# Kernel optimization log

Measured on AMD Instinct MI355X. Metric: run time of the kernel, lower is better.

The kernel has to match this reference:

```python
import jax, jax.numpy as jnp
import numpy as np

D_MODEL, JOINT_DIM, VOCAB = 512, 640, 1024
B, T, U = 4, 256, 64


def setup_inputs() -> dict:
    key = jax.random.key(0)
    ks = jax.random.split(key, 8)
    s_in = 1.0 / np.sqrt(D_MODEL)
    s_j = 1.0 / np.sqrt(JOINT_DIM)
    return {
        "enc": jax.random.normal(ks[0], (B, T, D_MODEL), jnp.float32),
        "pred": jax.random.normal(ks[1], (B, U, D_MODEL), jnp.float32),
        "enc_w": jax.random.uniform(ks[2], (JOINT_DIM, D_MODEL), jnp.float32, -s_in, s_in),
        "enc_b": jax.random.uniform(ks[3], (JOINT_DIM,), jnp.float32, -s_in, s_in),
        "pred_w": jax.random.uniform(ks[4], (JOINT_DIM, D_MODEL), jnp.float32, -s_in, s_in),
        "pred_b": jax.random.uniform(ks[5], (JOINT_DIM,), jnp.float32, -s_in, s_in),
        "out_w": jax.random.uniform(ks[6], (VOCAB, JOINT_DIM), jnp.float32, -s_j, s_j),
        "out_b": jax.random.uniform(ks[7], (VOCAB,), jnp.float32, -s_j, s_j),
    }


def reference(enc, pred, enc_w, enc_b, pred_w, pred_b, out_w, out_b):
    # project encoder (B,T,J) and predictor (B,U,J)
    e = jnp.einsum("btd,jd->btj", enc, enc_w) + enc_b
    p = jnp.einsum("bud,jd->buj", pred, pred_w) + pred_b
    # broadcast add over the (T,U) grid, tanh, then vocab projection
    z = jnp.tanh(e[:, :, None, :] + p[:, None, :, :])  # (B,T,U,J)
    logits = jnp.einsum("btuj,vj->btuv", z, out_w) + out_b  # (B,T,U,V)
    return logits
```

## Files before the change

kernel.cpp:

```cpp
#include <hip/hip_runtime.h>
#include <cstdint>
#include <cstddef>


typedef __attribute__((ext_vector_type(8))) __bf16 bf16x8;
typedef __attribute__((ext_vector_type(4))) float f32x4;

__device__ __forceinline__ int swz(int row, int kElem) {
  return (row << 6) + (kElem ^ ((row & 7) << 3));
}

__device__ __forceinline__ float fast_tanh(float x) {
  float e = __builtin_amdgcn_exp2f(x * 2.88539008177793f);
  return 1.0f - 2.0f * __builtin_amdgcn_rcpf(e + 1.0f);
}

__device__ __forceinline__ void gload_lds16(const void* g, void* l) {
  __builtin_amdgcn_global_load_lds(
      (const __attribute__((address_space(1))) void*)g,
      (__attribute__((address_space(3))) void*)l, 16, 0, 0);
}

__device__ void proj_tile(const float* __restrict__ A, const float* __restrict__ W,
                          const float* __restrict__ bias, __bf16* __restrict__ C,
                          int mt, int nt, __bf16* As, __bf16* Bs)
{
  const int tid  = threadIdx.x;
  const int r = tid & 127, half = tid >> 7;
  const int lane = tid & 63, wv = tid >> 6;
  const int wm = wv >> 1, wn = wv & 1;

  const float* arow = A + (size_t)(mt * 128 + r) * 512 + half * 32;
  const float* wrow = W + (size_t)(nt * 128 + r) * 512 + half * 32;

  f32x4 acc[4][4] = {};

  for (int k0 = 0; k0 < 512; k0 += 64) {
#pragma unroll
    for (int s = 0; s < 4; ++s) {
      f32x4 a0 = *(const f32x4*)(arow + k0 + s * 8);
      f32x4 a1 = *(const f32x4*)(arow + k0 + s * 8 + 4);
      f32x4 w0 = *(const f32x4*)(wrow + k0 + s * 8);
      f32x4 w1 = *(const f32x4*)(wrow + k0 + s * 8 + 4);
      bf16x8 za, zw;
#pragma unroll
      for (int j = 0; j < 4; ++j) {
        za[j] = (__bf16)a0[j]; za[4 + j] = (__bf16)a1[j];
        zw[j] = (__bf16)w0[j]; zw[4 + j] = (__bf16)w1[j];
      }
      const int kk = half * 32 + s * 8;
      *(bf16x8*)&As[swz(r, kk)] = za;
      *(bf16x8*)&Bs[swz(r, kk)] = zw;
    }
    __syncthreads();
#pragma unroll
    for (int kk = 0; kk < 2; ++kk) {
      bf16x8 af[4], bfr[4];
#pragma unroll
      for (int i = 0; i < 4; ++i) {
        af[i]  = *(const bf16x8*)&As[swz(wm * 64 + i * 16 + (lane & 15), kk * 32 + (lane >> 4) * 8)];
        bfr[i] = *(const bf16x8*)&Bs[swz(wn * 64 + i * 16 + (lane & 15), kk * 32 + (lane >> 4) * 8)];
      }
#pragma unroll
      for (int mi = 0; mi < 4; ++mi)
#pragma unroll
        for (int ni = 0; ni < 4; ++ni)
          acc[mi][ni] = __builtin_amdgcn_mfma_f32_16x16x32_bf16(af[mi], bfr[ni], acc[mi][ni], 0, 0, 0);
    }
    __syncthreads();
  }

  const int rowbase = mt * 128 + wm * 64;
  const int colbase = nt * 128 + wn * 64;
#pragma unroll
  for (int ni = 0; ni < 4; ++ni) {
    const int col = colbase + ni * 16 + (lane & 15);
    const float bb = bias[col];
#pragma unroll
    for (int mi = 0; mi < 4; ++mi) {
      const int row = rowbase + mi * 16 + (lane >> 4) * 4;
#pragma unroll
      for (int rg = 0; rg < 4; ++rg)
        C[(size_t)(row + rg) * 640 + col] = (__bf16)(acc[mi][ni][rg] + bb);
    }
  }
}

__global__ __launch_bounds__(256) void prep_kernel(
    const float* __restrict__ enc,  const float* __restrict__ enc_w,  const float* __restrict__ enc_b,
    const float* __restrict__ pred, const float* __restrict__ pred_w, const float* __restrict__ pred_b,
    const float* __restrict__ out_w,
    __bf16* __restrict__ E, __bf16* __restrict__ P, __bf16* __restrict__ Wb)
{
  __shared__ __align__(16) __bf16 As[128 * 64];
  __shared__ __align__(16) __bf16 Bs[128 * 64];
  const int bid = blockIdx.x;
  if (bid < 40) {
    proj_tile(enc, enc_w, enc_b, E, bid / 5, bid % 5, As, Bs);
  } else if (bid < 50) {
    proj_tile(pred, pred_w, pred_b, P, (bid - 40) / 5, (bid - 40) % 5, As, Bs);
  } else {
    const int gid = (bid - 50) * 256 + threadIdx.x;
    const int v  = gid / 80;
    const int j8 = gid % 80;
    f32x4 w0 = *(const f32x4*)(out_w + (size_t)v * 640 + j8 * 8);
    f32x4 w1 = *(const f32x4*)(out_w + (size_t)v * 640 + j8 * 8 + 4);
    bf16x8 z;
#pragma unroll
    for (int j = 0; j < 4; ++j) { z[j] = (__bf16)w0[j]; z[4 + j] = (__bf16)w1[j]; }
    const int nb = v >> 7, rr = v & 127;
    const int kb = j8 >> 3, kk = (j8 & 7) * 8;
    *(bf16x8*)(Wb + ((size_t)(nb * 10 + kb) << 13) + swz(rr, kk)) = z;
  }
}

__global__ __launch_bounds__(256) void zprod_kernel(
    const __bf16* __restrict__ E, const __bf16* __restrict__ P,
    __bf16* __restrict__ Z)
{
  const int bid = blockIdx.x;
  const int mt = bid / 10, kt = bid % 10;
  const int row0 = mt << 7;
  const int b  = row0 >> 14;
  const int t0 = (row0 >> 6) & 255;
  __bf16* zdst = Z + ((size_t)bid << 13);
  const int k0 = kt << 6;

#pragma unroll
  for (int c = 0; c < 4; ++c) {
    const int o = c * 2048 + threadIdx.x * 8;
    const int r = o >> 6;
    const int k = (o & 63) ^ ((r & 7) << 3);
    const __bf16* ep = E + (size_t)((b << 8) + t0 + (r >> 6)) * 640 + k0 + k;
    const __bf16* pp = P + (size_t)((b << 6) + (r & 63)) * 640 + k0 + k;
    bf16x8 e8 = *(const bf16x8*)ep;
    bf16x8 p8 = *(const bf16x8*)pp;
    bf16x8 z;
#pragma unroll
    for (int j = 0; j < 8; ++j)
      z[j] = (__bf16)fast_tanh((float)e8[j] + (float)p8[j]);
    *(bf16x8*)&zdst[o] = z;
  }
}

__global__ __launch_bounds__(256) void joiner_mainz(
    const __bf16* __restrict__ Z, const __bf16* __restrict__ Wb,
    const float* __restrict__ outb, float* __restrict__ out)
{
  __shared__ __align__(16) __bf16 As[8192];
  __shared__ __align__(16) __bf16 Bs[8192];
  const int wg = blockIdx.x;
  const int bid = (wg & 7) * 512 + (wg >> 3);
  const int mt = bid >> 3, nt = bid & 7;
  const int tid = threadIdx.x;
  const int lane = tid & 63, wv = tid >> 6;
  const int wm = wv >> 1, wn = wv & 1;

  const __bf16* zsrc = Z  + ((size_t)(mt * 10) << 13);
  const __bf16* wsrc = Wb + ((size_t)(nt * 10) << 13);

  f32x4 acc[4][4] = {};

  for (int kt = 0; kt < 10; ++kt) {
    const size_t kb = (size_t)kt << 13;
#pragma unroll
    for (int c = 0; c < 4; ++c) {
      const int off = c * 2048 + wv * 512;
      gload_lds16(zsrc + kb + off + lane * 8, &As[off]);
      gload_lds16(wsrc + kb + off + lane * 8, &Bs[off]);
    }
    __syncthreads();
#pragma unroll
    for (int kk = 0; kk < 2; ++kk) {
      bf16x8 af[4], bfr[4];
#pragma unroll
      for (int i = 0; i < 4; ++i) {
        af[i]  = *(const bf16x8*)&As[swz(wm * 64 + i * 16 + (lane & 15), kk * 32 + (lane >> 4) * 8)];
        bfr[i] = *(const bf16x8*)&Bs[swz(wn * 64 + i * 16 + (lane & 15), kk * 32 + (lane >> 4) * 8)];
      }
#pragma unroll
      for (int mi = 0; mi < 4; ++mi)
#pragma unroll
        for (int ni = 0; ni < 4; ++ni)
          acc[mi][ni] = __builtin_amdgcn_mfma_f32_16x16x32_bf16(af[mi], bfr[ni], acc[mi][ni], 0, 0, 0);
    }
    __syncthreads();
  }

  const int rowbase = (mt << 7) + wm * 64;
  const int colbase = (nt << 7) + wn * 64;
#pragma unroll
  for (int ni = 0; ni < 4; ++ni) {
    const int col = colbase + ni * 16 + (lane & 15);
    const float bb = outb[col];
#pragma unroll
    for (int mi = 0; mi < 4; ++mi) {
      const int row = rowbase + mi * 16 + (lane >> 4) * 4;
#pragma unroll
      for (int rg = 0; rg < 4; ++rg)
        out[(size_t)(row + rg) * 1024 + col] = acc[mi][ni][rg] + bb;
    }
  }
}

__global__ __launch_bounds__(512, 4) void joiner_fused(
    const __bf16* __restrict__ E, const __bf16* __restrict__ P,
    const __bf16* __restrict__ Wb, const float* __restrict__ outb,
    float* __restrict__ out)
{
  __shared__ __align__(16) __bf16 As[8192];
  __shared__ __align__(16) __bf16 Bs[2][16384];
  const int tid = threadIdx.x;
  const int nt = blockIdx.x & 3;
  const int mt = blockIdx.x >> 2;
  const int row0 = mt << 7;
  const int b  = row0 >> 14;
  const int t0 = (row0 >> 6) & 255;
  const int ar = tid & 127, h = tid >> 7;
  const int lane = tid & 63, wv = tid >> 6;
  const int wm = wv >> 2, wn = wv & 3;

  const __bf16* ep = E + (size_t)((b << 8) + t0 + (ar >> 6)) * 640 + h * 16;
  const __bf16* pp = P + (size_t)((b << 6) + (ar & 63)) * 640 + h * 16;

  f32x4 acc[4][4] = {};
  bf16x8 eA[2], pA[2];

  auto stageB = [&](int kt, __bf16* dst) {
#pragma unroll
    for (int c = 0; c < 4; ++c) {
      const int blk = nt * 2 + (c >> 1);
      const int off = (c & 1) * 4096 + wv * 512;
      gload_lds16(Wb + ((size_t)(blk * 10 + kt) << 13) + off + lane * 8,
                  dst + c * 2048 * 2 - (c >> 1) * 8192 + ((c & 1) * 4096 + wv * 512) - ((c & 1) * 4096 + wv * 512) + (c * 4096 - (c >> 1) * 8192) * 0 + 0);
    }
  };
  (void)stageB;

  auto stageB2 = [&](int kt, __bf16* dst) {
#pragma unroll
    for (int c = 0; c < 4; ++c) {
      const int blk = nt * 2 + (c >> 1);
      const int inoff = (c & 1) * 4096 + wv * 512;
      gload_lds16(Wb + ((size_t)(blk * 10 + kt) << 13) + inoff + lane * 8,
                  dst + (c >> 1) * 8192 + inoff);
    }
  };
  auto loadEP = [&](int k0) {
#pragma unroll
    for (int c = 0; c < 2; ++c) {
      eA[c] = *(const bf16x8*)(ep + k0 + c * 8);
      pA[c] = *(const bf16x8*)(pp + k0 + c * 8);
    }
  };
  auto writeA = [&]() {
#pragma unroll
    for (int c = 0; c < 2; ++c) {
      bf16x8 z;
#pragma unroll
      for (int j = 0; j < 8; ++j)
        z[j] = (__bf16)fast_tanh((float)eA[c][j] + (float)pA[c][j]);
      *(bf16x8*)&As[swz(ar, h * 16 + c * 8)] = z;
    }
  };
  auto compute = [&](const __bf16* Bsc) {
#pragma unroll
    for (int kk = 0; kk < 2; ++kk) {
      bf16x8 af[4], bfr[4];
#pragma unroll
      for (int i = 0; i < 4; ++i) {
        af[i]  = *(const bf16x8*)&As[swz(wm * 64 + i * 16 + (lane & 15), kk * 32 + (lane >> 4) * 8)];
        bfr[i] = *(const bf16x8*)&Bsc[swz(wn * 64 + i * 16 + (lane & 15), kk * 32 + (lane >> 4) * 8)];
      }
      asm volatile("s_waitcnt lgkmcnt(0)" ::: "memory");
      __builtin_amdgcn_sched_barrier(0);
      __builtin_amdgcn_s_setprio(1);
#pragma unroll
      for (int mi = 0; mi < 4; ++mi)
#pragma unroll
        for (int ni = 0; ni < 4; ++ni)
          acc[mi][ni] = __builtin_amdgcn_mfma_f32_16x16x32_bf16(af[mi], bfr[ni], acc[mi][ni], 0, 0, 0);
      __builtin_amdgcn_s_setprio(0);
    }
  };

  stageB2(0, Bs[0]);
  loadEP(0);
  writeA();
  asm volatile("s_waitcnt vmcnt(0) lgkmcnt(0)" ::: "memory");
  __builtin_amdgcn_s_barrier();

  for (int kt = 0; kt < 9; ++kt) {
    const int cur = kt & 1;
    stageB2(kt + 1, Bs[cur ^ 1]);
    loadEP((kt + 1) << 6);
    compute(Bs[cur]);
    __builtin_amdgcn_s_barrier();
    __builtin_amdgcn_sched_barrier(0);
    writeA();
    asm volatile("s_waitcnt lgkmcnt(0)" ::: "memory");
    __builtin_amdgcn_s_barrier();
  }
  compute(Bs[1]);

  const int rowbase = row0 + wm * 64;
  const int colbase = (nt << 8) + wn * 64;
#pragma unroll
  for (int ni = 0; ni < 4; ++ni) {
    const int col = colbase + ni * 16 + (lane & 15);
    const float bb = outb[col];
#pragma unroll
    for (int mi = 0; mi < 4; ++mi) {
      const int row = rowbase + mi * 16 + (lane >> 4) * 4;
#pragma unroll
      for (int rg = 0; rg < 4; ++rg)
        out[(size_t)(row + rg) * 1024 + col] = acc[mi][ni][rg] + bb;
    }
  }
}

extern "C" void kernel_launch(void* const* d_in, const int* in_sizes, int n_in,
                              void* d_out, int out_size, void* d_ws, size_t ws_size,
                              hipStream_t stream) {
  const float* enc    = (const float*)d_in[0];
  const float* pred   = (const float*)d_in[1];
  const float* enc_w  = (const float*)d_in[2];
  const float* enc_b  = (const float*)d_in[3];
  const float* pred_w = (const float*)d_in[4];
  const float* pred_b = (const float*)d_in[5];
  const float* out_w  = (const float*)d_in[6];
  const float* out_b  = (const float*)d_in[7];
  float* out = (float*)d_out;

  char* ws = (char*)d_ws;
  __bf16* E  = (__bf16*)(ws);
  __bf16* P  = (__bf16*)(ws + 1310720);
  __bf16* Wb = (__bf16*)(ws + 1638400);
  __bf16* Z  = (__bf16*)(ws + 2949120);

  prep_kernel<<<dim3(370), dim3(256), 0, stream>>>(
      enc, enc_w, enc_b, pred, pred_w, pred_b, out_w, E, P, Wb);

  if (ws_size >= (size_t)86835200) {
    zprod_kernel<<<dim3(5120), dim3(256), 0, stream>>>(E, P, Z);
    joiner_mainz<<<dim3(4096), dim3(256), 0, stream>>>(Z, Wb, out_b, out);
  } else {
    joiner_fused<<<dim3(2048), dim3(512), 0, stream>>>(E, P, Wb, out_b, out);
  }
}
```

Baseline: 171.7 us.

## Replace Z-path GEMM with 256x256-tile, 4-stage LDS ring pipelined kernel

```diff
diff --git a/kernel.cpp b/kernel.cpp
--- a/kernel.cpp
+++ b/kernel.cpp
@@ -6,8 +6,11 @@
 typedef __attribute__((ext_vector_type(8))) __bf16 bf16x8;
 typedef __attribute__((ext_vector_type(4))) float f32x4;
 
-__device__ __forceinline__ int swz(int row, int kElem) {
+__device__ __forceinline__ int swz64(int row, int kElem) {
   return (row << 6) + (kElem ^ ((row & 7) << 3));
+}
+__device__ __forceinline__ int swz32(int row, int kElem) {
+  return (row << 5) + ((kElem & 7) | (((kElem >> 3) ^ ((row >> 2) & 3)) << 3));
 }
 
 __device__ __forceinline__ float fast_tanh(float x) {
@@ -49,8 +52,8 @@
         zw[j] = (__bf16)w0[j]; zw[4 + j] = (__bf16)w1[j];
       }
       const int kk = half * 32 + s * 8;
-      *(bf16x8*)&As[swz(r, kk)] = za;
-      *(bf16x8*)&Bs[swz(r, kk)] = zw;
+      *(bf16x8*)&As[swz64(r, kk)] = za;
+      *(bf16x8*)&Bs[swz64(r, kk)] = zw;
     }
     __syncthreads();
 #pragma unroll
@@ -58,8 +61,8 @@
       bf16x8 af[4], bfr[4];
 #pragma unroll
       for (int i = 0; i < 4; ++i) {
-        af[i]  = *(const bf16x8*)&As[swz(wm * 64 + i * 16 + (lane & 15), kk * 32 + (lane >> 4) * 8)];
-        bfr[i] = *(const bf16x8*)&Bs[swz(wn * 64 + i * 16 + (lane & 15), kk * 32 + (lane >> 4) * 8)];
+        af[i]  = *(const bf16x8*)&As[swz64(wm * 64 + i * 16 + (lane & 15), kk * 32 + (lane >> 4) * 8)];
+        bfr[i] = *(const bf16x8*)&Bs[swz64(wn * 64 + i * 16 + (lane & 15), kk * 32 + (lane >> 4) * 8)];
       }
 #pragma unroll
       for (int mi = 0; mi < 4; ++mi)
@@ -90,7 +93,7 @@
     const float* __restrict__ enc,  const float* __restrict__ enc_w,  const float* __restrict__ enc_b,
     const float* __restrict__ pred, const float* __restrict__ pred_w, const float* __restrict__ pred_b,
     const float* __restrict__ out_w,
-    __bf16* __restrict__ E, __bf16* __restrict__ P, __bf16* __restrict__ Wb)
+    __bf16* __restrict__ E, __bf16* __restrict__ P, __bf16* __restrict__ Wb, int zpath)
 {
   __shared__ __align__(16) __bf16 As[128 * 64];
   __shared__ __align__(16) __bf16 Bs[128 * 64];
@@ -108,9 +111,15 @@
     bf16x8 z;
 #pragma unroll
     for (int j = 0; j < 4; ++j) { z[j] = (__bf16)w0[j]; z[4 + j] = (__bf16)w1[j]; }
-    const int nb = v >> 7, rr = v & 127;
-    const int kb = j8 >> 3, kk = (j8 & 7) * 8;
-    *(bf16x8*)(Wb + ((size_t)(nb * 10 + kb) << 13) + swz(rr, kk)) = z;
+    if (zpath) {
+      const int nb = v >> 8, rr = v & 255;
+      const int kt = j8 >> 2;
+      *(bf16x8*)(Wb + ((size_t)(nb * 20 + kt) << 13) + swz32(rr, (j8 & 3) * 8)) = z;
+    } else {
+      const int nb = v >> 7, rr = v & 127;
+      const int kb = j8 >> 3, kk = (j8 & 7) * 8;
+      *(bf16x8*)(Wb + ((size_t)(nb * 10 + kb) << 13) + swz64(rr, kk)) = z;
+    }
   }
 }
 
@@ -119,20 +128,20 @@
     __bf16* __restrict__ Z)
 {
   const int bid = blockIdx.x;
-  const int mt = bid / 10, kt = bid % 10;
-  const int row0 = mt << 7;
+  const int mt = bid / 20, kt = bid % 20;
+  const int row0 = mt << 8;
   const int b  = row0 >> 14;
   const int t0 = (row0 >> 6) & 255;
   __bf16* zdst = Z + ((size_t)bid << 13);
-  const int k0 = kt << 6;
 
 #pragma unroll
   for (int c = 0; c < 4; ++c) {
     const int o = c * 2048 + threadIdx.x * 8;
-    const int r = o >> 6;
-    const int k = (o & 63) ^ ((r & 7) << 3);
-    const __bf16* ep = E + (size_t)((b << 8) + t0 + (r >> 6)) * 640 + k0 + k;
-    const __bf16* pp = P + (size_t)((b << 6) + (r & 63)) * 640 + k0 + k;
+    const int r = o >> 5;
+    const int cc = (o >> 3) & 3;
+    const int k = kt * 32 + ((cc ^ ((r >> 2) & 3)) << 3);
+    const __bf16* ep = E + (size_t)((b << 8) + t0 + (r >> 6)) * 640 + k;
+    const __bf16* pp = P + (size_t)((b << 6) + (r & 63)) * 640 + k;
     bf16x8 e8 = *(const bf16x8*)ep;
     bf16x8 p8 = *(const bf16x8*)pp;
     bf16x8 z;
@@ -143,58 +152,77 @@
   }
 }
 
-__global__ __launch_bounds__(256) void joiner_mainz(
+__global__ __launch_bounds__(512, 2) void joiner_ring(
     const __bf16* __restrict__ Z, const __bf16* __restrict__ Wb,
     const float* __restrict__ outb, float* __restrict__ out)
 {
-  __shared__ __align__(16) __bf16 As[8192];
-  __shared__ __align__(16) __bf16 Bs[8192];
+  __shared__ __align__(16) __bf16 As[4][8192];
+  __shared__ __align__(16) __bf16 Bs[4][8192];
   const int wg = blockIdx.x;
-  const int bid = (wg & 7) * 512 + (wg >> 3);
-  const int mt = bid >> 3, nt = bid & 7;
+  const int bid = (wg & 7) * 128 + (wg >> 3);
+  const int mt = bid >> 2, nt = bid & 3;
   const int tid = threadIdx.x;
   const int lane = tid & 63, wv = tid >> 6;
-  const int wm = wv >> 1, wn = wv & 1;
-
-  const __bf16* zsrc = Z  + ((size_t)(mt * 10) << 13);
-  const __bf16* wsrc = Wb + ((size_t)(nt * 10) << 13);
-
-  f32x4 acc[4][4] = {};
-
-  for (int kt = 0; kt < 10; ++kt) {
-    const size_t kb = (size_t)kt << 13;
-#pragma unroll
-    for (int c = 0; c < 4; ++c) {
-      const int off = c * 2048 + wv * 512;
-      gload_lds16(zsrc + kb + off + lane * 8, &As[off]);
-      gload_lds16(wsrc + kb + off + lane * 8, &Bs[off]);
-    }
-    __syncthreads();
-#pragma unroll
-    for (int kk = 0; kk < 2; ++kk) {
-      bf16x8 af[4], bfr[4];
-#pragma unroll
-      for (int i = 0; i < 4; ++i) {
-        af[i]  = *(const bf16x8*)&As[swz(wm * 64 + i * 16 + (lane & 15), kk * 32 + (lane >> 4) * 8)];
-        bfr[i] = *(const bf16x8*)&Bs[swz(wn * 64 + i * 16 + (lane & 15), kk * 32 + (lane >> 4) * 8)];
-      }
-#pragma unroll
-      for (int mi = 0; mi < 4; ++mi)
-#pragma unroll
-        for (int ni = 0; ni < 4; ++ni)
-          acc[mi][ni] = __builtin_amdgcn_mfma_f32_16x16x32_bf16(af[mi], bfr[ni], acc[mi][ni], 0, 0, 0);
-    }
-    __syncthreads();
-  }
-
-  const int rowbase = (mt << 7) + wm * 64;
-  const int colbase = (nt << 7) + wn * 64;
+  const int wm = wv >> 2, wn = wv & 3;
+
+  const __bf16* zsrc = Z  + ((size_t)(mt * 20) << 13);
+  const __bf16* wsrc = Wb + ((size_t)(nt * 20) << 13);
+
+  f32x4 acc[8][4] = {};
+
+  const int arow_s = ((wm * 128 + (lane & 15)) >> 2) & 3;
+  const int brow_s = ((wn * 64  + (lane & 15)) >> 2) & 3;
+  const int aoff = (wm * 128 + (lane & 15)) * 32 + (((lane >> 4) ^ arow_s) << 3);
+  const int boff = (wn * 64  + (lane & 15)) * 32 + (((lane >> 4) ^ brow_s) << 3);
+
+  auto stage = [&](int t) {
+    const int s = t & 3;
+    const size_t g = (size_t)t << 13;
+#pragma unroll
+    for (int c = 0; c < 2; ++c) {
+      const int off = c * 4096 + wv * 512;
+      gload_lds16(zsrc + g + off + lane * 8, &As[s][off]);
+      gload_lds16(wsrc + g + off + lane * 8, &Bs[s][off]);
+    }
+  };
+
+  stage(0); stage(1); stage(2);
+  asm volatile("s_waitcnt vmcnt(8)" ::: "memory");
+  __builtin_amdgcn_s_barrier();
+
+#pragma unroll
+  for (int t = 0; t < 20; ++t) {
+    const int s = t & 3;
+    if (t < 17) stage(t + 3);
+    __builtin_amdgcn_s_setprio(1);
+    bf16x8 bfr[4];
+#pragma unroll
+    for (int ni = 0; ni < 4; ++ni)
+      bfr[ni] = *(const bf16x8*)&Bs[s][boff + ni * 512];
+#pragma unroll
+    for (int mi = 0; mi < 8; ++mi) {
+      bf16x8 af = *(const bf16x8*)&As[s][aoff + mi * 512];
+#pragma unroll
+      for (int ni = 0; ni < 4; ++ni)
+        acc[mi][ni] = __builtin_amdgcn_mfma_f32_16x16x32_bf16(af, bfr[ni], acc[mi][ni], 0, 0, 0);
+    }
+    __builtin_amdgcn_s_setprio(0);
+    if (t < 19) {
+      if (t < 17)       asm volatile("s_waitcnt vmcnt(8)" ::: "memory");
+      else if (t == 17) asm volatile("s_waitcnt vmcnt(4)" ::: "memory");
+      else              asm volatile("s_waitcnt vmcnt(0)" ::: "memory");
+      __builtin_amdgcn_s_barrier();
+    }
+  }
+
+  const int rowbase = (mt << 8) + wm * 128;
+  const int colbase = (nt << 8) + wn * 64;
 #pragma unroll
   for (int ni = 0; ni < 4; ++ni) {
     const int col = colbase + ni * 16 + (lane & 15);
     const float bb = outb[col];
 #pragma unroll
-    for (int mi = 0; mi < 4; ++mi) {
+    for (int mi = 0; mi < 8; ++mi) {
       const int row = rowbase + mi * 16 + (lane >> 4) * 4;
 #pragma unroll
       for (int rg = 0; rg < 4; ++rg)
@@ -226,17 +254,6 @@
   f32x4 acc[4][4] = {};
   bf16x8 eA[2], pA[2];
 
-  auto stageB = [&](int kt, __bf16* dst) {
-#pragma unroll
-    for (int c = 0; c < 4; ++c) {
-      const int blk = nt * 2 + (c >> 1);
-      const int off = (c & 1) * 4096 + wv * 512;
-      gload_lds16(Wb + ((size_t)(blk * 10 + kt) << 13) + off + lane * 8,
-                  dst + c * 2048 * 2 - (c >> 1) * 8192 + ((c & 1) * 4096 + wv * 512) - ((c & 1) * 4096 + wv * 512) + (c * 4096 - (c >> 1) * 8192) * 0 + 0);
-    }
-  };
-  (void)stageB;
-
   auto stageB2 = [&](int kt, __bf16* dst) {
 #pragma unroll
     for (int c = 0; c < 4; ++c) {
@@ -260,7 +277,7 @@
 #pragma unroll
       for (int j = 0; j < 8; ++j)
         z[j] = (__bf16)fast_tanh((float)eA[c][j] + (float)pA[c][j]);
-      *(bf16x8*)&As[swz(ar, h * 16 + c * 8)] = z;
+      *(bf16x8*)&As[swz64(ar, h * 16 + c * 8)] = z;
     }
   };
   auto compute = [&](const __bf16* Bsc) {
@@ -269,8 +286,8 @@
       bf16x8 af[4], bfr[4];
 #pragma unroll
       for (int i = 0; i < 4; ++i) {
-        af[i]  = *(const bf16x8*)&As[swz(wm * 64 + i * 16 + (lane & 15), kk * 32 + (lane >> 4) * 8)];
-        bfr[i] = *(const bf16x8*)&Bsc[swz(wn * 64 + i * 16 + (lane & 15), kk * 32 + (lane >> 4) * 8)];
+        af[i]  = *(const bf16x8*)&As[swz64(wm * 64 + i * 16 + (lane & 15), kk * 32 + (lane >> 4) * 8)];
+        bfr[i] = *(const bf16x8*)&Bsc[swz64(wn * 64 + i * 16 + (lane & 15), kk * 32 + (lane >> 4) * 8)];
       }
       asm volatile("s_waitcnt lgkmcnt(0)" ::: "memory");
       __builtin_amdgcn_sched_barrier(0);
@@ -338,12 +355,14 @@
   __bf16* Wb = (__bf16*)(ws + 1638400);
   __bf16* Z  = (__bf16*)(ws + 2949120);
 
+  const int zpath = (ws_size >= (size_t)86835200) ? 1 : 0;
+
   prep_kernel<<<dim3(370), dim3(256), 0, stream>>>(
-      enc, enc_w, enc_b, pred, pred_w, pred_b, out_w, E, P, Wb);
-
-  if (ws_size >= (size_t)86835200) {
+      enc, enc_w, enc_b, pred, pred_w, pred_b, out_w, E, P, Wb, zpath);
+
+  if (zpath) {
     zprod_kernel<<<dim3(5120), dim3(256), 0, stream>>>(E, P, Z);
-    joiner_mainz<<<dim3(4096), dim3(256), 0, stream>>>(Z, Wb, out_b, out);
+    joiner_ring<<<dim3(1024), dim3(512), 0, stream>>>(Z, Wb, out_b, out);
   } else {
     joiner_fused<<<dim3(2048), dim3(512), 0, stream>>>(E, P, Wb, out_b, out);
   }
```

Measured after the change: 173.2 us. Within noise of the previous version (+0.9%).
